# Performance work log

Hardware: AMD Instinct MI355X
Metric: run time of the kernel (lower is better)

Reference implementation:

```python
import jax, jax.numpy as jnp
import numpy as np

# fixed ontology layer output sizes (edge_index[-1].max()+1 in the original)
NUM_OUT = (5000, 1000, 256)


def setup_inputs() -> dict:
    key = jax.random.key(0)
    ks = jax.random.split(key, 12)
    B, F0 = 1024, 20000
    sizes_in = (20000, 5000, 1000)
    n_edges = (100000, 50000, 10000)
    inp = {
        "data": jax.random.normal(ks[0], (B, F0), dtype=jnp.float32),
        "p0": jax.random.normal(ks[1], (sizes_in[0],), dtype=jnp.float32),
        "p1": jax.random.normal(ks[2], (sizes_in[1],), dtype=jnp.float32),
        "p2": jax.random.normal(ks[3], (sizes_in[2],), dtype=jnp.float32),
        "W": jax.random.normal(ks[4], (10, NUM_OUT[-1]), dtype=jnp.float32) * (2.0 / (10 + NUM_OUT[-1])) ** 0.5,
        "b": jnp.zeros((10,), dtype=jnp.float32),
    }
    rng = np.random.default_rng(0)
    for i, (nin, nout, ne) in enumerate(zip(sizes_in, NUM_OUT, n_edges)):
        src = rng.integers(0, nin, size=ne).astype(np.int32)
        dst = rng.integers(0, nout, size=ne).astype(np.int32)
        dst[:nout] = np.arange(nout, dtype=np.int32)  # ensure every output node gets >=1 edge
        inp[f"src{i}"] = jnp.asarray(src)
        inp[f"dst{i}"] = jnp.asarray(dst)
    return inp


def _layer(x, p, src, dst, num_out):
    # elementwise scale -> gather along feature dim -> scatter-mean -> relu
    t = x * p  # [B, Fin]
    lifted = t[:, src]  # [B, E]
    sums = jnp.zeros((x.shape[0], num_out), x.dtype).at[:, dst].add(lifted)
    cnt = jnp.zeros((num_out,), x.dtype).at[dst].add(1.0)
    return jax.nn.relu(sums / jnp.maximum(cnt, 1.0))


def reference(data, p0, p1, p2, W, b, src0, dst0, src1, dst1, src2, dst2):
    x = _layer(data, p0, src0, dst0, NUM_OUT[0])
    x = _layer(x, p1, src1, dst1, NUM_OUT[1])
    x = _layer(x, p2, src2, dst2, NUM_OUT[2])
    out = x @ W.T + b  # Linear(256, 10)
    return jnp.squeeze(out, -1) if out.shape[-1] == 1 else out
```

## Files before the change

### kernel.cpp

```cpp
#include <hip/hip_runtime.h>
#include <hip/hip_fp16.h>

constexpr int Bsz   = 1024;
constexpr int F0    = 20000;
constexpr int NOUT0 = 5000, NOUT1 = 1000, NOUT2 = 256;
constexpr int NE0   = 100000, NE1 = 50000, NE2 = 10000;
constexpr int CNT_N  = NOUT0 + NOUT1 + NOUT2;
constexpr int OFFS_N = CNT_N + 3;
constexpr int CSR_N  = NE0 + NE1 + NE2;
constexpr int MAXIDX = 512;
constexpr int NTILE_F = (F0 + 63) / 64;
constexpr int NTILE   = NTILE_F * (Bsz / 64);
constexpr int SCB     = (CSR_N + 255) / 256;

union H4 { uint2 u; __half2 h[2]; };

__global__ __launch_bounds__(1024) void count_scan(
    const int* __restrict__ dst0, const int* __restrict__ dst1,
    const int* __restrict__ dst2, int* __restrict__ offs, int* __restrict__ cursor)
{
    __shared__ int cnt_lds[NOUT0];
    __shared__ int sc[1024];
    const int L = blockIdx.x;
    const int t = threadIdx.x;
    const int n  = (L == 0) ? NOUT0 : (L == 1) ? NOUT1 : NOUT2;
    const int ne = (L == 0) ? NE0   : (L == 1) ? NE1   : NE2;
    const int* dst = (L == 0) ? dst0 : (L == 1) ? dst1 : dst2;
    const int cb = (L == 0) ? 0 : (L == 1) ? NOUT0 : NOUT0 + NOUT1;
    const int ob = (L == 0) ? 0 : (L == 1) ? NOUT0 + 1 : NOUT0 + NOUT1 + 2;
    int* ofs = offs + ob;
    int* cur = cursor + cb;

    for (int i = t; i < n; i += 1024) cnt_lds[i] = 0;
    __syncthreads();
    for (int e = t; e < ne; e += 1024) atomicAdd(&cnt_lds[dst[e]], 1);
    __syncthreads();

    constexpr int CH = 5;
    const int base = t * CH;
    int vals[CH];
    int local = 0;
#pragma unroll
    for (int k = 0; k < CH; ++k) {
        const int i = base + k;
        const int v = (i < n) ? cnt_lds[i] : 0;
        vals[k] = v; local += v;
    }
    sc[t] = local;
    __syncthreads();
    for (int d = 1; d < 1024; d <<= 1) {
        const int v = (t >= d) ? sc[t - d] : 0;
        __syncthreads();
        sc[t] += v;
        __syncthreads();
    }
    int excl = sc[t] - local;
#pragma unroll
    for (int k = 0; k < CH; ++k) {
        const int i = base + k;
        if (i < n) { ofs[i] = excl; cur[i] = excl; }
        excl += vals[k];
    }
    if (t == 1023) ofs[n] = sc[1023];
}

__global__ __launch_bounds__(256) void transpose_scatter(
    const float* __restrict__ data, const float* __restrict__ p0,
    __half* __restrict__ dataT,
    const int* __restrict__ src0, const int* __restrict__ dst0,
    const int* __restrict__ src1, const int* __restrict__ dst1,
    const int* __restrict__ src2, const int* __restrict__ dst2,
    int* __restrict__ cursor, int* __restrict__ csr)
{
    const int t = threadIdx.x;
    const int bid = blockIdx.x;
    if (bid < NTILE) {
        __shared__ float tile[64][65];
        const int c0 = (bid % NTILE_F) * 64;
        const int r0 = (bid / NTILE_F) * 64;
        const int f4 = t & 15, rr = t >> 4;
        const int col = c0 + f4 * 4;
        if (col < F0) {
#pragma unroll
            for (int p = 0; p < 4; ++p) {
                const int br = rr + p * 16;
                const float4 v = *(const float4*)&data[(size_t)(r0 + br) * F0 + col];
                tile[br][f4 * 4 + 0] = v.x; tile[br][f4 * 4 + 1] = v.y;
                tile[br][f4 * 4 + 2] = v.z; tile[br][f4 * 4 + 3] = v.w;
            }
        }
        __syncthreads();
        const int b4 = t & 15, fr = t >> 4;
#pragma unroll
        for (int p = 0; p < 4; ++p) {
            const int f = c0 + fr + p * 16;
            if (f < F0) {
                const float s = p0[f];
                H4 o;
                o.h[0] = __floats2half2_rn(tile[b4 * 4 + 0][fr + p * 16] * s,
                                           tile[b4 * 4 + 1][fr + p * 16] * s);
                o.h[1] = __floats2half2_rn(tile[b4 * 4 + 2][fr + p * 16] * s,
                                           tile[b4 * 4 + 3][fr + p * 16] * s);
                *(uint2*)&dataT[(size_t)f * Bsz + r0 + b4 * 4] = o.u;
            }
        }
    } else {
        const int i = (bid - NTILE) * 256 + t;
        if (i < NE0) {
            const int pos = atomicAdd(&cursor[dst0[i]], 1);
            csr[pos] = src0[i];
        } else if (i < NE0 + NE1) {
            const int k = i - NE0;
            const int pos = atomicAdd(&cursor[NOUT0 + dst1[k]], 1);
            csr[NE0 + pos] = src1[k];
        } else if (i < CSR_N) {
            const int k = i - NE0 - NE1;
            const int pos = atomicAdd(&cursor[NOUT0 + NOUT1 + dst2[k]], 1);
            csr[NE0 + NE1 + pos] = src2[k];
        }
    }
}

__global__ __launch_bounds__(256) void layer_fwd(
    const __half* __restrict__ xT, const int* __restrict__ csr,
    const int* __restrict__ offs, const float* __restrict__ pnext,
    __half* __restrict__ yT)
{
    __shared__ int sidx[MAXIDX];
    const int j = blockIdx.x;
    const int t = threadIdx.x;
    const int beg = offs[j], end = offs[j + 1];
    const int n = end - beg;
    const int np = n < MAXIDX ? n : MAXIDX;
    for (int i = t; i < np; i += 256) sidx[i] = csr[beg + i];
    __syncthreads();

    const int c = t * 4;
    float4 a0 = make_float4(0.f, 0.f, 0.f, 0.f);
    float4 a1 = make_float4(0.f, 0.f, 0.f, 0.f);
    int e = 0;
    for (; e + 2 <= np; e += 2) {
        H4 u0, u1;
        u0.u = *(const uint2*)&xT[(size_t)sidx[e + 0] * Bsz + c];
        u1.u = *(const uint2*)&xT[(size_t)sidx[e + 1] * Bsz + c];
        const float2 f00 = __half22float2(u0.h[0]);
        const float2 f01 = __half22float2(u0.h[1]);
        const float2 f10 = __half22float2(u1.h[0]);
        const float2 f11 = __half22float2(u1.h[1]);
        a0.x += f00.x; a0.y += f00.y; a0.z += f01.x; a0.w += f01.y;
        a1.x += f10.x; a1.y += f10.y; a1.z += f11.x; a1.w += f11.y;
    }
    if (e < np) {
        H4 u; u.u = *(const uint2*)&xT[(size_t)sidx[e] * Bsz + c];
        const float2 f0 = __half22float2(u.h[0]);
        const float2 f1 = __half22float2(u.h[1]);
        a0.x += f0.x; a0.y += f0.y; a0.z += f1.x; a0.w += f1.y;
    }
    for (int ee = MAXIDX; ee < n; ++ee) {
        H4 u; u.u = *(const uint2*)&xT[(size_t)csr[beg + ee] * Bsz + c];
        const float2 f0 = __half22float2(u.h[0]);
        const float2 f1 = __half22float2(u.h[1]);
        a0.x += f0.x; a0.y += f0.y; a0.z += f1.x; a0.w += f1.y;
    }
    a0.x += a1.x; a0.y += a1.y; a0.z += a1.z; a0.w += a1.w;

    const float inv = 1.0f / fmaxf((float)n, 1.0f);
    const float sc = (pnext ? pnext[j] : 1.0f) * inv;
    H4 o;
    o.h[0] = __floats2half2_rn(fmaxf(a0.x, 0.f) * sc, fmaxf(a0.y, 0.f) * sc);
    o.h[1] = __floats2half2_rn(fmaxf(a0.z, 0.f) * sc, fmaxf(a0.w, 0.f) * sc);
    *(uint2*)&yT[(size_t)j * Bsz + c] = o.u;
}

__global__ __launch_bounds__(256) void head_gemm(
    const __half* __restrict__ y2T, const float* __restrict__ W,
    const float* __restrict__ bias, float* __restrict__ out)
{
    __shared__ float ws[10 * 256];
    __shared__ float bs[10];
    const int t = threadIdx.x;
    for (int i = t; i < 10 * 256; i += 256) ws[i] = W[i];
    if (t < 10) bs[t] = bias[t];
    __syncthreads();

    const int b = blockIdx.x * 256 + t;
    float acc[10];
#pragma unroll
    for (int o = 0; o < 10; ++o) acc[o] = bs[o];
    for (int k = 0; k < 256; ++k) {
        const float v = __half2float(y2T[(size_t)k * Bsz + b]);
#pragma unroll
        for (int o = 0; o < 10; ++o) acc[o] += v * ws[o * 256 + k];
    }
#pragma unroll
    for (int o = 0; o < 10; ++o) out[(size_t)b * 10 + o] = acc[o];
}

extern "C" void kernel_launch(void* const* d_in, const int* in_sizes, int n_in,
                              void* d_out, int out_size, void* d_ws, size_t ws_size,
                              hipStream_t stream)
{
    const float* data = (const float*)d_in[0];
    const float* p0   = (const float*)d_in[1];
    const float* p1   = (const float*)d_in[2];
    const float* p2   = (const float*)d_in[3];
    const float* W    = (const float*)d_in[4];
    const float* bias = (const float*)d_in[5];
    const int* src0 = (const int*)d_in[6];
    const int* dst0 = (const int*)d_in[7];
    const int* src1 = (const int*)d_in[8];
    const int* dst1 = (const int*)d_in[9];
    const int* src2 = (const int*)d_in[10];
    const int* dst2 = (const int*)d_in[11];

    char* ws = (char*)d_ws;
    auto align = [](size_t x) { return (x + 255) & ~size_t(255); };
    size_t o = 0;
    __half* dataT = (__half*)(ws + o); o = align(o + (size_t)F0 * Bsz * 2);
    __half* y0    = (__half*)(ws + o); o = align(o + (size_t)NOUT0 * Bsz * 2);
    __half* y1    = (__half*)(ws + o); o = align(o + (size_t)NOUT1 * Bsz * 2);
    __half* y2    = (__half*)(ws + o); o = align(o + (size_t)NOUT2 * Bsz * 2);
    int* offs     = (int*)(ws + o);    o = align(o + (size_t)OFFS_N * 4);
    int* cursor   = (int*)(ws + o);    o = align(o + (size_t)CNT_N * 4);
    int* csr      = (int*)(ws + o);    o = align(o + (size_t)CSR_N * 4);

    count_scan<<<3, 1024, 0, stream>>>(dst0, dst1, dst2, offs, cursor);
    transpose_scatter<<<NTILE + SCB, 256, 0, stream>>>(
        data, p0, dataT, src0, dst0, src1, dst1, src2, dst2, cursor, csr);
    layer_fwd<<<NOUT0, 256, 0, stream>>>(dataT, csr, offs, p1, y0);
    layer_fwd<<<NOUT1, 256, 0, stream>>>(y0, csr + NE0, offs + NOUT0 + 1, p2, y1);
    layer_fwd<<<NOUT2, 256, 0, stream>>>(y1, csr + NE0 + NE1, offs + NOUT0 + NOUT1 + 2,
                                         nullptr, y2);
    head_gemm<<<Bsz / 256, 256, 0, stream>>>(y2, W, bias, (float*)d_out);
}
```

Before: 143.7 us.

## Split each output node's gather-mean across eight batch slices of 64-thread blocks

The per-layer gather kernel now launches eight 64-thread blocks per output node, each covering a 128-column batch slice with half2 loads, instead of one 256-thread block covering the whole batch with 4-half loads. This raises the block count, which matters most for the small later layers (1000 and 256 nodes) where there were too few blocks to fill the GPU. The inner loop is unrolled four-wide with independent accumulators to keep more loads in flight. In exchange, every slice block reloads the CSR index list, the loads are narrower, and there are more but smaller blocks to schedule.

```diff
diff --git a/kernel.cpp b/kernel.cpp
--- a/kernel.cpp
+++ b/kernel.cpp
@@ -12,6 +12,8 @@
 constexpr int NTILE_F = (F0 + 63) / 64;
 constexpr int NTILE   = NTILE_F * (Bsz / 64);
 constexpr int SCB     = (CSR_N + 255) / 256;
+constexpr int NSLICE  = 8;
+constexpr int SLW     = Bsz / NSLICE;
 
 union H4 { uint2 u; __half2 h[2]; };
 
@@ -121,55 +123,54 @@
     }
 }
 
-__global__ __launch_bounds__(256) void layer_fwd(
+template<int LAYER>
+__global__ __launch_bounds__(64) void layer_slice(
     const __half* __restrict__ xT, const int* __restrict__ csr,
     const int* __restrict__ offs, const float* __restrict__ pnext,
     __half* __restrict__ yT)
 {
     __shared__ int sidx[MAXIDX];
-    const int j = blockIdx.x;
+    const int bid = blockIdx.x;
+    const int slice = bid & (NSLICE - 1);
+    const int j = bid >> 3;
     const int t = threadIdx.x;
     const int beg = offs[j], end = offs[j + 1];
     const int n = end - beg;
     const int np = n < MAXIDX ? n : MAXIDX;
-    for (int i = t; i < np; i += 256) sidx[i] = csr[beg + i];
-    __syncthreads();
-
-    const int c = t * 4;
-    float4 a0 = make_float4(0.f, 0.f, 0.f, 0.f);
-    float4 a1 = make_float4(0.f, 0.f, 0.f, 0.f);
+    for (int i = t; i < np; i += 64) sidx[i] = csr[beg + i];
+    __syncthreads();
+
+    const int c = slice * SLW + t * 2;
+    float a0x = 0.f, a0y = 0.f, a1x = 0.f, a1y = 0.f;
+    float a2x = 0.f, a2y = 0.f, a3x = 0.f, a3y = 0.f;
     int e = 0;
-    for (; e + 2 <= np; e += 2) {
-        H4 u0, u1;
-        u0.u = *(const uint2*)&xT[(size_t)sidx[e + 0] * Bsz + c];
-        u1.u = *(const uint2*)&xT[(size_t)sidx[e + 1] * Bsz + c];
-        const float2 f00 = __half22float2(u0.h[0]);
-        const float2 f01 = __half22float2(u0.h[1]);
-        const float2 f10 = __half22float2(u1.h[0]);
-        const float2 f11 = __half22float2(u1.h[1]);
-        a0.x += f00.x; a0.y += f00.y; a0.z += f01.x; a0.w += f01.y;
-        a1.x += f10.x; a1.y += f10.y; a1.z += f11.x; a1.w += f11.y;
-    }
-    if (e < np) {
-        H4 u; u.u = *(const uint2*)&xT[(size_t)sidx[e] * Bsz + c];
-        const float2 f0 = __half22float2(u.h[0]);
-        const float2 f1 = __half22float2(u.h[1]);
-        a0.x += f0.x; a0.y += f0.y; a0.z += f1.x; a0.w += f1.y;
+    for (; e + 4 <= np; e += 4) {
+        const __half2 v0 = *(const __half2*)&xT[(size_t)sidx[e + 0] * Bsz + c];
+        const __half2 v1 = *(const __half2*)&xT[(size_t)sidx[e + 1] * Bsz + c];
+        const __half2 v2 = *(const __half2*)&xT[(size_t)sidx[e + 2] * Bsz + c];
+        const __half2 v3 = *(const __half2*)&xT[(size_t)sidx[e + 3] * Bsz + c];
+        const float2 f0 = __half22float2(v0);
+        const float2 f1 = __half22float2(v1);
+        const float2 f2 = __half22float2(v2);
+        const float2 f3 = __half22float2(v3);
+        a0x += f0.x; a0y += f0.y; a1x += f1.x; a1y += f1.y;
+        a2x += f2.x; a2y += f2.y; a3x += f3.x; a3y += f3.y;
+    }
+    for (; e < np; ++e) {
+        const float2 f = __half22float2(*(const __half2*)&xT[(size_t)sidx[e] * Bsz + c]);
+        a0x += f.x; a0y += f.y;
     }
     for (int ee = MAXIDX; ee < n; ++ee) {
-        H4 u; u.u = *(const uint2*)&xT[(size_t)csr[beg + ee] * Bsz + c];
-        const float2 f0 = __half22float2(u.h[0]);
-        const float2 f1 = __half22float2(u.h[1]);
-        a0.x += f0.x; a0.y += f0.y; a0.z += f1.x; a0.w += f1.y;
-    }
-    a0.x += a1.x; a0.y += a1.y; a0.z += a1.z; a0.w += a1.w;
+        const float2 f = __half22float2(*(const __half2*)&xT[(size_t)csr[beg + ee] * Bsz + c]);
+        a0x += f.x; a0y += f.y;
+    }
+    const float ax = a0x + a1x + a2x + a3x;
+    const float ay = a0y + a1y + a2y + a3y;
 
     const float inv = 1.0f / fmaxf((float)n, 1.0f);
     const float sc = (pnext ? pnext[j] : 1.0f) * inv;
-    H4 o;
-    o.h[0] = __floats2half2_rn(fmaxf(a0.x, 0.f) * sc, fmaxf(a0.y, 0.f) * sc);
-    o.h[1] = __floats2half2_rn(fmaxf(a0.z, 0.f) * sc, fmaxf(a0.w, 0.f) * sc);
-    *(uint2*)&yT[(size_t)j * Bsz + c] = o.u;
+    const __half2 o = __floats2half2_rn(fmaxf(ax, 0.f) * sc, fmaxf(ay, 0.f) * sc);
+    *(__half2*)&yT[(size_t)j * Bsz + c] = o;
 }
 
 __global__ __launch_bounds__(256) void head_gemm(
@@ -227,9 +228,9 @@
     count_scan<<<3, 1024, 0, stream>>>(dst0, dst1, dst2, offs, cursor);
     transpose_scatter<<<NTILE + SCB, 256, 0, stream>>>(
         data, p0, dataT, src0, dst0, src1, dst1, src2, dst2, cursor, csr);
-    layer_fwd<<<NOUT0, 256, 0, stream>>>(dataT, csr, offs, p1, y0);
-    layer_fwd<<<NOUT1, 256, 0, stream>>>(y0, csr + NE0, offs + NOUT0 + 1, p2, y1);
-    layer_fwd<<<NOUT2, 256, 0, stream>>>(y1, csr + NE0 + NE1, offs + NOUT0 + NOUT1 + 2,
-                                         nullptr, y2);
+    layer_slice<0><<<NOUT0 * NSLICE, 64, 0, stream>>>(dataT, csr, offs, p1, y0);
+    layer_slice<1><<<NOUT1 * NSLICE, 64, 0, stream>>>(y0, csr + NE0, offs + NOUT0 + 1, p2, y1);
+    layer_slice<2><<<NOUT2 * NSLICE, 64, 0, stream>>>(y1, csr + NE0 + NE1,
+                                                      offs + NOUT0 + NOUT1 + 2, nullptr, y2);
     head_gemm<<<Bsz / 256, 256, 0, stream>>>(y2, W, bias, (float*)d_out);
 }
```

Result: faster. 125.0 us (-13.0%).
